# Kernel tuning notes

Hardware: AMD Instinct MI355X
Metric: run time of the kernel (lower is better)

The kernel has to match this reference:

```python
import jax, jax.numpy as jnp
import numpy as np

N = 4096        # sequence length
H = 16          # heads
D_MODEL = 1024
D_HEAD = D_MODEL // H  # 64


def setup_inputs() -> dict:
    key = jax.random.key(0)
    ks = jax.random.split(key, 9)
    scale = 1.0 / np.sqrt(D_MODEL)
    inp = {
        "X_Q": jax.random.normal(ks[0], (N, D_MODEL), dtype=jnp.float32),
        "X_K": jax.random.normal(ks[1], (N, D_MODEL), dtype=jnp.float32),
        "X_V": jax.random.normal(ks[2], (N, D_MODEL), dtype=jnp.float32),
        # per-head projection weights, stacked over head axis: [H, D_MODEL, D_HEAD]
        "Wq": jax.random.normal(ks[3], (H, D_MODEL, D_HEAD), dtype=jnp.float32) * scale,
        "bq": jax.random.normal(ks[4], (H, D_HEAD), dtype=jnp.float32) * scale,
        "Wk": jax.random.normal(ks[5], (H, D_MODEL, D_HEAD), dtype=jnp.float32) * scale,
        "bk": jax.random.normal(ks[6], (H, D_HEAD), dtype=jnp.float32) * scale,
        "Wv": jax.random.normal(ks[7], (H, D_MODEL, D_HEAD), dtype=jnp.float32) * scale,
        "bv": jax.random.normal(ks[8], (H, D_HEAD), dtype=jnp.float32) * scale,
    }
    return inp


def reference(X_Q, X_K, X_V, Wq, bq, Wk, bk, Wv, bv):
    # Batched per-head projections (replaces the Python loop of nn.Linear calls)
    Q = jnp.einsum("nd,hdk->hnk", X_Q, Wq) + bq[:, None, :]   # [H, N, D_HEAD]
    K = jnp.einsum("nd,hdk->hnk", X_K, Wk) + bk[:, None, :]
    V = jnp.einsum("nd,hdk->hnk", X_V, Wv) + bv[:, None, :]
    scores = jnp.einsum("hnk,hmk->hnm", Q, K) / jnp.sqrt(jnp.float32(D_HEAD))  # [H, N, N]
    attn = jax.nn.softmax(scores, axis=-1)  # softmax over keys (dim=1 of the [n,n] per-head matrix)
    out = jnp.einsum("hnm,hmv->hnv", attn, V)  # [H, N, D_HEAD]
    # concat heads along feature dim -> [N, D_MODEL]
    return jnp.transpose(out, (1, 0, 2)).reshape(N, D_MODEL)
```

## Files before the change

### kernel.cpp

```cpp
#include <hip/hip_runtime.h>

typedef unsigned short u16;
typedef __attribute__((ext_vector_type(8))) short bf16x8;
typedef __attribute__((ext_vector_type(16))) float floatx16;

#define C2 0.18033688011112042f
#define TRUNC_BIAS 0.99859f

static __device__ __forceinline__ u16 f2b(float f) {
  unsigned u = __builtin_bit_cast(unsigned, f);
  u = (u + 0x7FFFu + ((u >> 16) & 1u)) >> 16;
  return (u16)u;
}
static __device__ __forceinline__ unsigned pk2(float a, float b) {
  return (unsigned)f2b(a) | ((unsigned)f2b(b) << 16);
}
static __device__ __forceinline__ void gl_lds16(const void* g, void* l) {
  __builtin_amdgcn_global_load_lds(
      (const __attribute__((address_space(1))) unsigned*)g,
      (__attribute__((address_space(3))) unsigned*)l, 16, 0, 0);
}
static __device__ __forceinline__ float ex2(float x) {
#if __has_builtin(__builtin_amdgcn_exp2f)
  return __builtin_amdgcn_exp2f(x);
#else
  return exp2f(x);
#endif
}
static __device__ __forceinline__ unsigned pkt(float a, float b) {
#if __has_builtin(__builtin_amdgcn_perm)
  return __builtin_amdgcn_perm(__builtin_bit_cast(unsigned, a),
                               __builtin_bit_cast(unsigned, b), 0x03020706u);
#else
  return (__builtin_bit_cast(unsigned, a) >> 16) |
         (__builtin_bit_cast(unsigned, b) & 0xffff0000u);
#endif
}
static __device__ __forceinline__ void pswap(unsigned& a, unsigned& b) {
#if __has_builtin(__builtin_amdgcn_permlane32_swap)
  auto r = __builtin_amdgcn_permlane32_swap(a, b, false, false);
  a = r[0];
  b = r[1];
#else
  unsigned ta = (unsigned)__shfl_xor((int)a, 32);
  unsigned tb = (unsigned)__shfl_xor((int)b, 32);
  bool hi = (threadIdx.x & 32) != 0;
  unsigned na = hi ? tb : a;
  unsigned nb = hi ? b : ta;
  a = na;
  b = nb;
#endif
}

__global__ __launch_bounds__(256) void convx_k(
    const float* __restrict__ x0, const float* __restrict__ x1, const float* __restrict__ x2,
    u16* __restrict__ o0, u16* __restrict__ o1, u16* __restrict__ o2) {
  int z = blockIdx.z;
  const float* x = z == 0 ? x0 : (z == 1 ? x1 : x2);
  u16* o = z == 0 ? o0 : (z == 1 ? o1 : o2);
  size_t i = ((size_t)blockIdx.x * 256 + threadIdx.x) * 8;
  float4 a = *(const float4*)(x + i);
  float4 b = *(const float4*)(x + i + 4);
  uint4 u;
  u.x = pk2(a.x, a.y); u.y = pk2(a.z, a.w);
  u.z = pk2(b.x, b.y); u.w = pk2(b.z, b.w);
  *(uint4*)(o + i) = u;
}

__global__ __launch_bounds__(256) void convw_k(
    const float* __restrict__ w0, const float* __restrict__ w1, const float* __restrict__ w2,
    u16* __restrict__ o0, u16* __restrict__ o1, u16* __restrict__ o2) {
  int z = blockIdx.z;
  const float* W = z == 0 ? w0 : (z == 1 ? w1 : w2);
  u16* O = z == 0 ? o0 : (z == 1 ? o1 : o2);
  int h = blockIdx.x >> 4, d0 = (blockIdx.x & 15) * 64;
  __shared__ __align__(16) float tile[64 * 68];
  int t = threadIdx.x;
  {
    int r = t >> 2, c = t & 3;
    const float* src = W + (size_t)h * 65536 + (size_t)(d0 + r) * 64 + c * 16;
#pragma unroll
    for (int i = 0; i < 4; ++i) {
      float4 v = *(const float4*)(src + 4 * i);
      *(float4*)&tile[r * 68 + c * 16 + 4 * i] = v;
    }
  }
  __syncthreads();
  {
    int k = t >> 2, dc = t & 3;
    unsigned u[8];
#pragma unroll
    for (int i = 0; i < 8; ++i) {
      float a = tile[(dc * 16 + 2 * i) * 68 + k];
      float b = tile[(dc * 16 + 2 * i + 1) * 68 + k];
      u[i] = pk2(a, b);
    }
    u16* dst = O + ((size_t)(h * 64 + k)) * 1024 + d0 + dc * 16;
    *(uint4*)dst = make_uint4(u[0], u[1], u[2], u[3]);
    *(uint4*)(dst + 8) = make_uint4(u[4], u[5], u[6], u[7]);
  }
}

__global__ __launch_bounds__(256, 3) void proj_k(
    const u16* __restrict__ x0, const u16* __restrict__ x1, const u16* __restrict__ x2,
    const u16* __restrict__ w0, const u16* __restrict__ w1, const u16* __restrict__ w2,
    const float* __restrict__ b0, const float* __restrict__ b1, const float* __restrict__ b2,
    u16* __restrict__ q0, u16* __restrict__ q1, u16* __restrict__ q2) {
  int z = blockIdx.z;
  const u16* X = z == 0 ? x0 : (z == 1 ? x1 : x2);
  const u16* Wt = z == 0 ? w0 : (z == 1 ? w1 : w2);
  const float* bias = z == 0 ? b0 : (z == 1 ? b1 : b2);
  u16* out = z == 0 ? q0 : (z == 1 ? q1 : q2);

  __shared__ uint4 smem4[32768 / 16];
  char* sm = (char*)smem4;
  const int t = threadIdx.x, lane = t & 63, wid = t >> 6;
  const int L = lane & 31, h2 = lane >> 5;
  const int wm = wid >> 1, wc = wid & 1;
  const int rowt = blockIdx.x + 8 * (blockIdx.y & 3);
  const int colt = blockIdx.y >> 2;
  const int n0 = rowt * 128, c0 = colt * 128;

  floatx16 acc[2][2];
#pragma unroll
  for (int a = 0; a < 2; ++a)
#pragma unroll
    for (int b = 0; b < 2; ++b)
#pragma unroll
      for (int r = 0; r < 16; ++r) acc[a][b][r] = 0.f;

  const int srow = t >> 3, sc8 = t & 7;
  for (int k0 = 0; k0 < 1024; k0 += 64) {
#pragma unroll
    for (int i = 0; i < 4; ++i) {
      int row = i * 32 + srow;
      int cg = sc8 ^ (row & 7);
      gl_lds16(X + (size_t)(n0 + row) * 1024 + k0 + cg * 8, sm + i * 4096 + t * 16);
    }
#pragma unroll
    for (int i = 0; i < 4; ++i) {
      int row = i * 32 + srow;
      int cg = sc8 ^ (row & 7);
      gl_lds16(Wt + (size_t)(c0 + row) * 1024 + k0 + cg * 8, sm + 16384 + i * 4096 + t * 16);
    }
    __syncthreads();
#pragma unroll
    for (int ks = 0; ks < 4; ++ks) {
      bf16x8 af[2], bfr[2];
#pragma unroll
      for (int mt = 0; mt < 2; ++mt) {
        int m = wm * 64 + mt * 32 + L;
        int cc = (2 * ks + h2) ^ (m & 7);
        af[mt] = *(const bf16x8*)(sm + m * 128 + cc * 16);
      }
#pragma unroll
      for (int ct = 0; ct < 2; ++ct) {
        int c = wc * 64 + ct * 32 + L;
        int cc = (2 * ks + h2) ^ (c & 7);
        bfr[ct] = *(const bf16x8*)(sm + 16384 + c * 128 + cc * 16);
      }
#pragma unroll
      for (int mt = 0; mt < 2; ++mt)
#pragma unroll
        for (int ct = 0; ct < 2; ++ct)
          acc[mt][ct] = __builtin_amdgcn_mfma_f32_32x32x16_bf16(af[mt], bfr[ct], acc[mt][ct], 0, 0, 0);
    }
    __syncthreads();
  }

  if (z == 0) {
#pragma unroll
    for (int ct = 0; ct < 2; ++ct) {
      int gcol = c0 + wc * 64 + ct * 32 + L;
      float bv = bias[gcol];
      int h = gcol >> 6, cl = gcol & 63;
#pragma unroll
      for (int mt = 0; mt < 2; ++mt)
#pragma unroll
        for (int r = 0; r < 16; ++r) {
          int seq = n0 + wm * 64 + mt * 32 + (r & 3) + 8 * (r >> 2) + 4 * h2;
          out[((size_t)h * 4096 + seq) * 64 + cl] = f2b((acc[mt][ct][r] + bv) * C2);
        }
    }
  } else if (z == 1) {
#pragma unroll
    for (int ct = 0; ct < 2; ++ct) {
      int gcol = c0 + wc * 64 + ct * 32 + L;
      float bv = bias[gcol];
      int h = gcol >> 6;
      int d = ct * 32 + L;
      int ks = d >> 4, h2k = (d >> 3) & 1, j = d & 7;
#pragma unroll
      for (int mt = 0; mt < 2; ++mt) {
        int T = (n0 + wm * 64 + mt * 32) >> 5;
        u16* baseT = out + (size_t)h * 262144 + ((size_t)T << 11) + ks * 512 + h2k * 256 + j;
#pragma unroll
        for (int r = 0; r < 16; ++r) {
          int Lk = (r & 3) + 8 * (r >> 2) + 4 * h2;
          baseT[Lk * 8] = f2b(acc[mt][ct][r] + bv);
        }
      }
    }
  } else {
#pragma unroll
    for (int ct = 0; ct < 2; ++ct) {
      int gcol = c0 + wc * 64 + ct * 32 + L;
      float bv = bias[gcol];
      int h = gcol >> 6;
#pragma unroll
      for (int mt = 0; mt < 2; ++mt) {
        int T = (n0 + wm * 64 + mt * 32) >> 5;
        unsigned pk[8];
#pragma unroll
        for (int g = 0; g < 8; ++g)
          pk[g] = pk2(acc[mt][ct][2 * g] + bv, acc[mt][ct][2 * g + 1] + bv);
        pswap(pk[0], pk[2]);
        pswap(pk[1], pk[3]);
        pswap(pk[4], pk[6]);
        pswap(pk[5], pk[7]);
        u16* basep = out + (size_t)h * 262144 + ((size_t)T << 11) + h2 * 256 + L * 8;
        *(uint4*)(basep + (ct * 2 + 0) * 512) = make_uint4(pk[0], pk[1], pk[2], pk[3]);
        *(uint4*)(basep + (ct * 2 + 1) * 512) = make_uint4(pk[4], pk[5], pk[6], pk[7]);
      }
    }
  }
}

__global__ __launch_bounds__(256, 2) void attn_k(
    const u16* __restrict__ Q, const u16* __restrict__ Kp, const u16* __restrict__ Vp,
    float* __restrict__ out) {
  __shared__ __align__(16) float Ob[2][64 * 68];
  __shared__ float lstat[4][64];
  const int t = threadIdx.x, lane = t & 63, w = t >> 6;
  const int L = lane & 31, h2 = lane >> 5;
  const int ws = w & 1, kh = w >> 1;
  const int h = blockIdx.x & 15, qt = blockIdx.x >> 4;
  const int n0 = qt * 128 + ws * 64;
  const u16* Qg = Q + (size_t)h * 4096 * 64;
  const u16* Kph = Kp + (size_t)h * 262144;
  const u16* Vph = Vp + (size_t)h * 262144;
  const int tbase = kh * 64;

  bf16x8 qf[2][4];
#pragma unroll
  for (int nt = 0; nt < 2; ++nt)
#pragma unroll
    for (int ks = 0; ks < 4; ++ks)
      qf[nt][ks] = *(const bf16x8*)(Qg + ((size_t)(n0 + nt * 32 + L)) * 64 + ks * 16 + h2 * 8);

  const floatx16 FZ = {0.f, 0.f, 0.f, 0.f, 0.f, 0.f, 0.f, 0.f,
                       0.f, 0.f, 0.f, 0.f, 0.f, 0.f, 0.f, 0.f};
  floatx16 accO[2][2];
#pragma unroll
  for (int a = 0; a < 2; ++a)
#pragma unroll
    for (int b = 0; b < 2; ++b) accO[a][b] = FZ;
  float l_run[2] = {0.f, 0.f};

  bf16x8 kfA[4], kfB[4], vfA[4], vfB[4];
  auto loadK = [&](int rn, bf16x8* kf) {
    const u16* p = Kph + ((size_t)(tbase + rn) << 11) + lane * 8;
#pragma unroll
    for (int ks = 0; ks < 4; ++ks) kf[ks] = *(const bf16x8*)(p + ks * 512);
  };
  auto loadV = [&](int rn, bf16x8* vf) {
    const u16* p = Vph + ((size_t)(tbase + rn) << 11) + lane * 8;
#pragma unroll
    for (int idx = 0; idx < 4; ++idx) vf[idx] = *(const bf16x8*)(p + idx * 512);
  };
  loadK(0, kfA);
  loadV(0, vfA);

  auto round = [&](int r, bf16x8* kf, bf16x8* vf, bf16x8* kfn, bf16x8* vfn) {
    floatx16 accS[2];
    accS[0] = __builtin_amdgcn_mfma_f32_32x32x16_bf16(kf[0], qf[0][0], FZ, 0, 0, 0);
    accS[1] = __builtin_amdgcn_mfma_f32_32x32x16_bf16(kf[0], qf[1][0], FZ, 0, 0, 0);
#pragma unroll
    for (int ks = 1; ks < 4; ++ks) {
      accS[0] = __builtin_amdgcn_mfma_f32_32x32x16_bf16(kf[ks], qf[0][ks], accS[0], 0, 0, 0);
      accS[1] = __builtin_amdgcn_mfma_f32_32x32x16_bf16(kf[ks], qf[1][ks], accS[1], 0, 0, 0);
    }
    int rn = (r + 1) & 63;
    loadK(rn, kfn);
    loadV(rn, vfn);

    unsigned pkr[2][8];
#pragma unroll
    for (int nt = 0; nt < 2; ++nt) {
      float p[16];
      float ss = 0.f;
#pragma unroll
      for (int q = 0; q < 16; ++q) {
        p[q] = ex2(accS[nt][q]);
        ss += p[q];
      }
      l_run[nt] += ss;
#pragma unroll
      for (int g = 0; g < 8; ++g) pkr[nt][g] = pkt(p[2 * g], p[2 * g + 1]);
      pswap(pkr[nt][0], pkr[nt][2]);
      pswap(pkr[nt][1], pkr[nt][3]);
      pswap(pkr[nt][4], pkr[nt][6]);
      pswap(pkr[nt][5], pkr[nt][7]);
    }

#pragma unroll
    for (int c2 = 0; c2 < 2; ++c2) {
      bf16x8 pf[2];
#pragma unroll
      for (int nt = 0; nt < 2; ++nt) {
        uint4 u = make_uint4(pkr[nt][c2 * 4], pkr[nt][c2 * 4 + 1],
                             pkr[nt][c2 * 4 + 2], pkr[nt][c2 * 4 + 3]);
        pf[nt] = __builtin_bit_cast(bf16x8, u);
      }
#pragma unroll
      for (int vt = 0; vt < 2; ++vt) {
        accO[vt][0] = __builtin_amdgcn_mfma_f32_32x32x16_bf16(vf[vt * 2 + c2], pf[0], accO[vt][0], 0, 0, 0);
        accO[vt][1] = __builtin_amdgcn_mfma_f32_32x32x16_bf16(vf[vt * 2 + c2], pf[1], accO[vt][1], 0, 0, 0);
      }
    }
  };

  for (int r = 0; r < 64; r += 2) {
    round(r, kfA, vfA, kfB, vfB);
    round(r + 1, kfB, vfB, kfA, vfA);
  }

  l_run[0] += __shfl_xor(l_run[0], 32);
  l_run[1] += __shfl_xor(l_run[1], 32);
  if (h2 == 0) {
    lstat[w][L] = l_run[0];
    lstat[w][32 + L] = l_run[1];
  }
  if (kh == 1) {
#pragma unroll
    for (int vt = 0; vt < 2; ++vt)
#pragma unroll
      for (int nt = 0; nt < 2; ++nt)
#pragma unroll
        for (int g = 0; g < 4; ++g)
          *(float4*)&Ob[ws][(nt * 32 + L) * 68 + vt * 32 + 8 * g + 4 * h2] =
              make_float4(accO[vt][nt][4 * g], accO[vt][nt][4 * g + 1],
                          accO[vt][nt][4 * g + 2], accO[vt][nt][4 * g + 3]);
  }
  __syncthreads();
  if (kh == 0) {
    float scale[2];
#pragma unroll
    for (int nt = 0; nt < 2; ++nt)
      scale[nt] = 1.f / ((lstat[ws][nt * 32 + L] + lstat[ws + 2][nt * 32 + L]) * TRUNC_BIAS);
#pragma unroll
    for (int vt = 0; vt < 2; ++vt)
#pragma unroll
      for (int nt = 0; nt < 2; ++nt)
#pragma unroll
        for (int g = 0; g < 4; ++g) {
          float4 o = *(const float4*)&Ob[ws][(nt * 32 + L) * 68 + vt * 32 + 8 * g + 4 * h2];
          float4 res;
          res.x = (accO[vt][nt][4 * g] + o.x) * scale[nt];
          res.y = (accO[vt][nt][4 * g + 1] + o.y) * scale[nt];
          res.z = (accO[vt][nt][4 * g + 2] + o.z) * scale[nt];
          res.w = (accO[vt][nt][4 * g + 3] + o.w) * scale[nt];
          *(float4*)(out + ((size_t)(n0 + nt * 32 + L)) * 1024 + h * 64 + vt * 32 + 8 * g + 4 * h2) = res;
        }
  }
}

extern "C" void kernel_launch(void* const* d_in, const int* in_sizes, int n_in,
                              void* d_out, int out_size, void* d_ws, size_t ws_size,
                              hipStream_t stream) {
  const float* XQ = (const float*)d_in[0];
  const float* XK = (const float*)d_in[1];
  const float* XV = (const float*)d_in[2];
  const float* Wq = (const float*)d_in[3];
  const float* bq = (const float*)d_in[4];
  const float* Wk = (const float*)d_in[5];
  const float* bk = (const float*)d_in[6];
  const float* Wv = (const float*)d_in[7];
  const float* bv = (const float*)d_in[8];

  const size_t MB = 1024 * 1024;
  char* w = (char*)d_ws;
  u16* xqb = (u16*)(w + 0 * MB);
  u16* xkb = (u16*)(w + 8 * MB);
  u16* xvb = (u16*)(w + 16 * MB);
  u16* wtq = (u16*)(w + 24 * MB);
  u16* wtk = (u16*)(w + 26 * MB);
  u16* wtv = (u16*)(w + 28 * MB);
  u16* Qb = (u16*)(w + 32 * MB);
  u16* Kpk = (u16*)(w + 56 * MB);
  u16* Vpk = (u16*)(w + 64 * MB);

  convx_k<<<dim3(2048, 1, 3), 256, 0, stream>>>(XQ, XK, XV, xqb, xkb, xvb);
  convw_k<<<dim3(256, 1, 3), 256, 0, stream>>>(Wq, Wk, Wv, wtq, wtk, wtv);
  proj_k<<<dim3(8, 32, 3), 256, 0, stream>>>(xqb, xkb, xvb, wtq, wtk, wtv,
                                             bq, bk, bv, Qb, Kpk, Vpk);
  attn_k<<<dim3(512), 256, 0, stream>>>(Qb, Kpk, Vpk, (float*)d_out);
}
```

Baseline: 212.5 us.

## Halve attention query tile per wave to raise occupancy and block count

Each wave in the attention kernel now handles 32 query rows instead of 64, and the grid doubles from 512 to 1024 blocks with launch bounds raised to 4 blocks per CU. The double-buffered K/V register sets are replaced by a single buffer whose next tile is loaded inside the loop, which cuts register pressure. The aim is more resident waves and better latency hiding on the many CUs of the chip. In exchange each K/V tile is reused for half as many queries, doubling K/V global traffic, and the simpler prefetch overlaps less.

```diff
diff --git a/kernel.cpp b/kernel.cpp
--- a/kernel.cpp
+++ b/kernel.cpp
@@ -226,142 +226,106 @@
   }
 }
 
-__global__ __launch_bounds__(256, 2) void attn_k(
+__global__ __launch_bounds__(256, 4) void attn_k(
     const u16* __restrict__ Q, const u16* __restrict__ Kp, const u16* __restrict__ Vp,
     float* __restrict__ out) {
-  __shared__ __align__(16) float Ob[2][64 * 68];
-  __shared__ float lstat[4][64];
+  __shared__ __align__(16) float Ob[2][32 * 68];
+  __shared__ float lstat[4][32];
   const int t = threadIdx.x, lane = t & 63, w = t >> 6;
   const int L = lane & 31, h2 = lane >> 5;
   const int ws = w & 1, kh = w >> 1;
   const int h = blockIdx.x & 15, qt = blockIdx.x >> 4;
-  const int n0 = qt * 128 + ws * 64;
+  const int n0 = qt * 64 + ws * 32;
   const u16* Qg = Q + (size_t)h * 4096 * 64;
-  const u16* Kph = Kp + (size_t)h * 262144;
-  const u16* Vph = Vp + (size_t)h * 262144;
-  const int tbase = kh * 64;
-
-  bf16x8 qf[2][4];
-#pragma unroll
-  for (int nt = 0; nt < 2; ++nt)
-#pragma unroll
-    for (int ks = 0; ks < 4; ++ks)
-      qf[nt][ks] = *(const bf16x8*)(Qg + ((size_t)(n0 + nt * 32 + L)) * 64 + ks * 16 + h2 * 8);
+  const u16* Kph = Kp + (size_t)h * 262144 + (((size_t)kh * 64) << 11) + lane * 8;
+  const u16* Vph = Vp + (size_t)h * 262144 + (((size_t)kh * 64) << 11) + lane * 8;
+
+  bf16x8 qf[4];
+#pragma unroll
+  for (int ks = 0; ks < 4; ++ks)
+    qf[ks] = *(const bf16x8*)(Qg + ((size_t)(n0 + L)) * 64 + ks * 16 + h2 * 8);
 
   const floatx16 FZ = {0.f, 0.f, 0.f, 0.f, 0.f, 0.f, 0.f, 0.f,
                        0.f, 0.f, 0.f, 0.f, 0.f, 0.f, 0.f, 0.f};
-  floatx16 accO[2][2];
-#pragma unroll
-  for (int a = 0; a < 2; ++a)
-#pragma unroll
-    for (int b = 0; b < 2; ++b) accO[a][b] = FZ;
-  float l_run[2] = {0.f, 0.f};
-
-  bf16x8 kfA[4], kfB[4], vfA[4], vfB[4];
-  auto loadK = [&](int rn, bf16x8* kf) {
-    const u16* p = Kph + ((size_t)(tbase + rn) << 11) + lane * 8;
-#pragma unroll
-    for (int ks = 0; ks < 4; ++ks) kf[ks] = *(const bf16x8*)(p + ks * 512);
-  };
-  auto loadV = [&](int rn, bf16x8* vf) {
-    const u16* p = Vph + ((size_t)(tbase + rn) << 11) + lane * 8;
-#pragma unroll
-    for (int idx = 0; idx < 4; ++idx) vf[idx] = *(const bf16x8*)(p + idx * 512);
-  };
-  loadK(0, kfA);
-  loadV(0, vfA);
-
-  auto round = [&](int r, bf16x8* kf, bf16x8* vf, bf16x8* kfn, bf16x8* vfn) {
-    floatx16 accS[2];
-    accS[0] = __builtin_amdgcn_mfma_f32_32x32x16_bf16(kf[0], qf[0][0], FZ, 0, 0, 0);
-    accS[1] = __builtin_amdgcn_mfma_f32_32x32x16_bf16(kf[0], qf[1][0], FZ, 0, 0, 0);
-#pragma unroll
-    for (int ks = 1; ks < 4; ++ks) {
-      accS[0] = __builtin_amdgcn_mfma_f32_32x32x16_bf16(kf[ks], qf[0][ks], accS[0], 0, 0, 0);
-      accS[1] = __builtin_amdgcn_mfma_f32_32x32x16_bf16(kf[ks], qf[1][ks], accS[1], 0, 0, 0);
-    }
+  floatx16 accO[2];
+  accO[0] = FZ;
+  accO[1] = FZ;
+  float l_run = 0.f;
+
+  bf16x8 kf[4], vf[4];
+#pragma unroll
+  for (int ks = 0; ks < 4; ++ks) kf[ks] = *(const bf16x8*)(Kph + ks * 512);
+#pragma unroll
+  for (int idx = 0; idx < 4; ++idx) vf[idx] = *(const bf16x8*)(Vph + idx * 512);
+
+  for (int r = 0; r < 64; ++r) {
+    floatx16 accS;
+    accS = __builtin_amdgcn_mfma_f32_32x32x16_bf16(kf[0], qf[0], FZ, 0, 0, 0);
+#pragma unroll
+    for (int ks = 1; ks < 4; ++ks)
+      accS = __builtin_amdgcn_mfma_f32_32x32x16_bf16(kf[ks], qf[ks], accS, 0, 0, 0);
+
     int rn = (r + 1) & 63;
-    loadK(rn, kfn);
-    loadV(rn, vfn);
-
-    unsigned pkr[2][8];
-#pragma unroll
-    for (int nt = 0; nt < 2; ++nt) {
-      float p[16];
-      float ss = 0.f;
-#pragma unroll
-      for (int q = 0; q < 16; ++q) {
-        p[q] = ex2(accS[nt][q]);
-        ss += p[q];
-      }
-      l_run[nt] += ss;
-#pragma unroll
-      for (int g = 0; g < 8; ++g) pkr[nt][g] = pkt(p[2 * g], p[2 * g + 1]);
-      pswap(pkr[nt][0], pkr[nt][2]);
-      pswap(pkr[nt][1], pkr[nt][3]);
-      pswap(pkr[nt][4], pkr[nt][6]);
-      pswap(pkr[nt][5], pkr[nt][7]);
-    }
+    const u16* pK = Kph + ((size_t)rn << 11);
+#pragma unroll
+    for (int ks = 0; ks < 4; ++ks) kf[ks] = *(const bf16x8*)(pK + ks * 512);
+
+    float p[16];
+    float ss = 0.f;
+#pragma unroll
+    for (int q = 0; q < 16; ++q) {
+      p[q] = ex2(accS[q]);
+      ss += p[q];
+    }
+    l_run += ss;
+    unsigned pkr[8];
+#pragma unroll
+    for (int g = 0; g < 8; ++g) pkr[g] = pkt(p[2 * g], p[2 * g + 1]);
+    pswap(pkr[0], pkr[2]);
+    pswap(pkr[1], pkr[3]);
+    pswap(pkr[4], pkr[6]);
+    pswap(pkr[5], pkr[7]);
 
 #pragma unroll
     for (int c2 = 0; c2 < 2; ++c2) {
-      bf16x8 pf[2];
-#pragma unroll
-      for (int nt = 0; nt < 2; ++nt) {
-        uint4 u = make_uint4(pkr[nt][c2 * 4], pkr[nt][c2 * 4 + 1],
-                             pkr[nt][c2 * 4 + 2], pkr[nt][c2 * 4 + 3]);
-        pf[nt] = __builtin_bit_cast(bf16x8, u);
-      }
-#pragma unroll
-      for (int vt = 0; vt < 2; ++vt) {
-        accO[vt][0] = __builtin_amdgcn_mfma_f32_32x32x16_bf16(vf[vt * 2 + c2], pf[0], accO[vt][0], 0, 0, 0);
-        accO[vt][1] = __builtin_amdgcn_mfma_f32_32x32x16_bf16(vf[vt * 2 + c2], pf[1], accO[vt][1], 0, 0, 0);
-      }
-    }
-  };
-
-  for (int r = 0; r < 64; r += 2) {
-    round(r, kfA, vfA, kfB, vfB);
-    round(r + 1, kfB, vfB, kfA, vfA);
-  }
-
-  l_run[0] += __shfl_xor(l_run[0], 32);
-  l_run[1] += __shfl_xor(l_run[1], 32);
-  if (h2 == 0) {
-    lstat[w][L] = l_run[0];
-    lstat[w][32 + L] = l_run[1];
-  }
+      uint4 u = make_uint4(pkr[c2 * 4], pkr[c2 * 4 + 1], pkr[c2 * 4 + 2], pkr[c2 * 4 + 3]);
+      bf16x8 pf = __builtin_bit_cast(bf16x8, u);
+#pragma unroll
+      for (int vt = 0; vt < 2; ++vt)
+        accO[vt] = __builtin_amdgcn_mfma_f32_32x32x16_bf16(vf[vt * 2 + c2], pf, accO[vt], 0, 0, 0);
+    }
+
+    const u16* pV = Vph + ((size_t)rn << 11);
+#pragma unroll
+    for (int idx = 0; idx < 4; ++idx) vf[idx] = *(const bf16x8*)(pV + idx * 512);
+  }
+
+  l_run += __shfl_xor(l_run, 32);
+  if (h2 == 0) lstat[w][L] = l_run;
   if (kh == 1) {
 #pragma unroll
     for (int vt = 0; vt < 2; ++vt)
 #pragma unroll
-      for (int nt = 0; nt < 2; ++nt)
-#pragma unroll
-        for (int g = 0; g < 4; ++g)
-          *(float4*)&Ob[ws][(nt * 32 + L) * 68 + vt * 32 + 8 * g + 4 * h2] =
-              make_float4(accO[vt][nt][4 * g], accO[vt][nt][4 * g + 1],
-                          accO[vt][nt][4 * g + 2], accO[vt][nt][4 * g + 3]);
+      for (int g = 0; g < 4; ++g)
+        *(float4*)&Ob[ws][L * 68 + vt * 32 + 8 * g + 4 * h2] =
+            make_float4(accO[vt][4 * g], accO[vt][4 * g + 1],
+                        accO[vt][4 * g + 2], accO[vt][4 * g + 3]);
   }
   __syncthreads();
   if (kh == 0) {
-    float scale[2];
-#pragma unroll
-    for (int nt = 0; nt < 2; ++nt)
-      scale[nt] = 1.f / ((lstat[ws][nt * 32 + L] + lstat[ws + 2][nt * 32 + L]) * TRUNC_BIAS);
+    float scale = 1.f / ((lstat[ws][L] + lstat[ws + 2][L]) * TRUNC_BIAS);
 #pragma unroll
     for (int vt = 0; vt < 2; ++vt)
 #pragma unroll
-      for (int nt = 0; nt < 2; ++nt)
-#pragma unroll
-        for (int g = 0; g < 4; ++g) {
-          float4 o = *(const float4*)&Ob[ws][(nt * 32 + L) * 68 + vt * 32 + 8 * g + 4 * h2];
-          float4 res;
-          res.x = (accO[vt][nt][4 * g] + o.x) * scale[nt];
-          res.y = (accO[vt][nt][4 * g + 1] + o.y) * scale[nt];
-          res.z = (accO[vt][nt][4 * g + 2] + o.z) * scale[nt];
-          res.w = (accO[vt][nt][4 * g + 3] + o.w) * scale[nt];
-          *(float4*)(out + ((size_t)(n0 + nt * 32 + L)) * 1024 + h * 64 + vt * 32 + 8 * g + 4 * h2) = res;
-        }
+      for (int g = 0; g < 4; ++g) {
+        float4 o = *(const float4*)&Ob[ws][L * 68 + vt * 32 + 8 * g + 4 * h2];
+        float4 res;
+        res.x = (accO[vt][4 * g] + o.x) * scale;
+        res.y = (accO[vt][4 * g + 1] + o.y) * scale;
+        res.z = (accO[vt][4 * g + 2] + o.z) * scale;
+        res.w = (accO[vt][4 * g + 3] + o.w) * scale;
+        *(float4*)(out + ((size_t)(n0 + L)) * 1024 + h * 64 + vt * 32 + 8 * g + 4 * h2) = res;
+      }
   }
 }
 
@@ -394,5 +358,5 @@
   convw_k<<<dim3(256, 1, 3), 256, 0, stream>>>(Wq, Wk, Wv, wtq, wtk, wtv);
   proj_k<<<dim3(8, 32, 3), 256, 0, stream>>>(xqb, xkb, xvb, wtq, wtk, wtv,
                                              bq, bk, bv, Qb, Kpk, Vpk);
-  attn_k<<<dim3(512), 256, 0, stream>>>(Qb, Kpk, Vpk, (float*)d_out);
-}
+  attn_k<<<dim3(1024), 256, 0, stream>>>(Qb, Kpk, Vpk, (float*)d_out);
+}
```

New measurement: 221.6 us. +4.3%, slower.

## Software-pipeline QK MFMA one tile ahead of softmax and PV

Applied to the files above, without the earlier changes.

Restructures the attention inner loop so the QK^T MFMAs for the next key tile are issued before the exp/pack and PV MFMAs of the current tile, with K and V loads staggered between stages. The goal is to overlap the transcendental/VALU softmax work with matrix-core work and hide global load latency. It needs an extra pair of score accumulators, which raises register pressure, and the loads wrap modulo 64, so the final iterations fetch redundant tiles.

```diff
diff --git a/kernel.cpp b/kernel.cpp
--- a/kernel.cpp
+++ b/kernel.cpp
@@ -257,22 +257,20 @@
     for (int b = 0; b < 2; ++b) accO[a][b] = FZ;
   float l_run[2] = {0.f, 0.f};
 
+  floatx16 accSA[2], accSB[2];
   bf16x8 kfA[4], kfB[4], vfA[4], vfB[4];
   auto loadK = [&](int rn, bf16x8* kf) {
-    const u16* p = Kph + ((size_t)(tbase + rn) << 11) + lane * 8;
+    const u16* p = Kph + ((size_t)(tbase + (rn & 63)) << 11) + lane * 8;
 #pragma unroll
     for (int ks = 0; ks < 4; ++ks) kf[ks] = *(const bf16x8*)(p + ks * 512);
   };
   auto loadV = [&](int rn, bf16x8* vf) {
-    const u16* p = Vph + ((size_t)(tbase + rn) << 11) + lane * 8;
+    const u16* p = Vph + ((size_t)(tbase + (rn & 63)) << 11) + lane * 8;
 #pragma unroll
     for (int idx = 0; idx < 4; ++idx) vf[idx] = *(const bf16x8*)(p + idx * 512);
   };
-  loadK(0, kfA);
-  loadV(0, vfA);
-
-  auto round = [&](int r, bf16x8* kf, bf16x8* vf, bf16x8* kfn, bf16x8* vfn) {
-    floatx16 accS[2];
+
+  auto qk = [&](bf16x8* kf, floatx16* accS) {
     accS[0] = __builtin_amdgcn_mfma_f32_32x32x16_bf16(kf[0], qf[0][0], FZ, 0, 0, 0);
     accS[1] = __builtin_amdgcn_mfma_f32_32x32x16_bf16(kf[0], qf[1][0], FZ, 0, 0, 0);
 #pragma unroll
@@ -280,11 +278,9 @@
       accS[0] = __builtin_amdgcn_mfma_f32_32x32x16_bf16(kf[ks], qf[0][ks], accS[0], 0, 0, 0);
       accS[1] = __builtin_amdgcn_mfma_f32_32x32x16_bf16(kf[ks], qf[1][ks], accS[1], 0, 0, 0);
     }
-    int rn = (r + 1) & 63;
-    loadK(rn, kfn);
-    loadV(rn, vfn);
-
-    unsigned pkr[2][8];
+  };
+  unsigned pkr[2][8];
+  auto expack = [&](floatx16* accS) {
 #pragma unroll
     for (int nt = 0; nt < 2; ++nt) {
       float p[16];
@@ -302,7 +298,8 @@
       pswap(pkr[nt][4], pkr[nt][6]);
       pswap(pkr[nt][5], pkr[nt][7]);
     }
-
+  };
+  auto pv = [&](bf16x8* vf) {
 #pragma unroll
     for (int c2 = 0; c2 < 2; ++c2) {
       bf16x8 pf[2];
@@ -320,9 +317,23 @@
     }
   };
 
+  loadK(0, kfA);
+  loadV(0, vfA);
+  qk(kfA, accSA);
+  loadK(1, kfB);
+  loadV(1, vfB);
+
   for (int r = 0; r < 64; r += 2) {
-    round(r, kfA, vfA, kfB, vfB);
-    round(r + 1, kfB, vfB, kfA, vfA);
+    qk(kfB, accSB);
+    loadK(r + 2, kfA);
+    expack(accSA);
+    pv(vfA);
+    loadV(r + 2, vfA);
+    qk(kfA, accSA);
+    loadK(r + 3, kfB);
+    expack(accSB);
+    pv(vfB);
+    loadV(r + 3, vfB);
   }
 
   l_run[0] += __shfl_xor(l_run[0], 32);
```

After: 236.4 us. +11.2%, slower.
